# Kernel optimization log

Hardware: AMD Instinct MI355X
Metric: run time of the kernel (lower is better)

## Reference

```python
import jax, jax.numpy as jnp
import numpy as np

B, S, H = 1, 2048, 2048
NH, NKV, HD = 16, 2, 128
ROPE_THETA = 1000000.0
BF16 = jnp.bfloat16


def setup_inputs() -> dict:
    key = jax.random.key(0)
    ks = jax.random.split(key, 6)
    hidden_states = jax.random.normal(ks[0], (B, S, H), dtype=jnp.float32)
    # causal additive mask, 0 on/below diagonal, large negative above
    causal = jnp.tril(jnp.ones((S, S), dtype=bool))
    attention_mask = jnp.where(causal, 0.0, -1e9).astype(jnp.float32)[None, None, :, :]
    position_ids = jnp.arange(S, dtype=jnp.int32)[None, :]
    sc = 1.0 / np.sqrt(H)
    Wq = jax.random.normal(ks[1], (H, H), dtype=jnp.float32) * sc
    bq = jnp.zeros((H,), dtype=jnp.float32)
    Wk = jax.random.normal(ks[2], (H, NKV * HD), dtype=jnp.float32) * sc
    bk = jnp.zeros((NKV * HD,), dtype=jnp.float32)
    Wv = jax.random.normal(ks[3], (H, NKV * HD), dtype=jnp.float32) * sc
    bv = jnp.zeros((NKV * HD,), dtype=jnp.float32)
    Wo = jax.random.normal(ks[4], (H, H), dtype=jnp.float32) * sc
    return {"hidden_states": hidden_states, "attention_mask": attention_mask,
            "position_ids": position_ids, "Wq": Wq, "bq": bq, "Wk": Wk, "bk": bk,
            "Wv": Wv, "bv": bv, "Wo": Wo}


def _rope_tables(pos):
    # pos: [S] int. freqs: [HD//2]
    freqs = 1.0 / (ROPE_THETA ** (jnp.arange(0, HD, 2, dtype=jnp.float32) / HD))
    ang = pos.astype(jnp.float32)[:, None] * freqs[None, :]  # [S, HD//2]
    return jnp.cos(ang), jnp.sin(ang)


def _apply_rope(x, cos, sin):
    # x: [B,S,nheads,HD]; cos/sin: [S,HD//2] -> broadcast over heads
    c = cos[None, :, None, :]
    s = sin[None, :, None, :]
    x1, x2 = x[..., : HD // 2], x[..., HD // 2 :]
    return jnp.concatenate([x1 * c - x2 * s, x1 * s + x2 * c], axis=-1)


def reference(hidden_states, attention_mask, position_ids, Wq, bq, Wk, bk, Wv, bv, Wo):
    x = hidden_states.astype(BF16)
    # bf16 projections (flax Dense dtype=bfloat16)
    q = (x @ Wq.astype(BF16) + bq.astype(BF16)).reshape(B, S, NH, HD)
    k = (x @ Wk.astype(BF16) + bk.astype(BF16)).reshape(B, S, NKV, HD)
    v = (x @ Wv.astype(BF16) + bv.astype(BF16)).reshape(B, S, NKV, HD)
    cos, sin = _rope_tables(position_ids[0])
    q = _apply_rope(q.astype(jnp.float32), cos, sin).astype(jnp.float32)
    k = _apply_rope(k.astype(jnp.float32), cos, sin).astype(jnp.float32)
    cache_k, cache_v = k, v  # cache holds un-repeated kv (k post-rope, v bf16)
    rep = NH // NKV  # GQA repeat
    k = jnp.repeat(k, rep, axis=2)
    vr = jnp.repeat(v, rep, axis=2)
    # [B,NH,S,HD]
    qh = q.transpose(0, 2, 1, 3)
    kh = k.transpose(0, 2, 1, 3)
    vh = vr.transpose(0, 2, 1, 3).astype(jnp.float32)
    scale = 1.0 / jnp.sqrt(jnp.float32(HD))
    scores = jnp.einsum('bhqd,bhkd->bhqk', qh, kh) * scale + attention_mask
    probs = jnp.clip(jax.nn.softmax(scores.astype(jnp.float32), axis=-1), 1e-09, 1 - 1e-09)
    attn = jnp.einsum('bhqk,bhkd->bhqd', probs, vh)
    attn = attn.transpose(0, 2, 1, 3).reshape(B, S, H)
    out = (attn.astype(BF16) @ Wo.astype(BF16)).astype(jnp.float32)
    return out, cache_k, cache_v
```

## Files before the change

kernel.cpp:

```cpp
#include <hip/hip_runtime.h>
#include <hip/hip_bf16.h>
#include <math.h>

#define S_LEN 2048
#define HDIM  2048
#define N_H   16
#define N_KV  2
#define HD_   128
#define NQKV  2560

typedef __attribute__((ext_vector_type(8))) short bf16x8;
typedef __attribute__((ext_vector_type(4))) float f32x4;
typedef __attribute__((ext_vector_type(16))) float f32x16;

#define GLDS16(gsrc, ldst)                                                      \
  __builtin_amdgcn_global_load_lds(                                             \
      (const __attribute__((address_space(1))) void*)(gsrc),                    \
      (__attribute__((address_space(3))) void*)(ldst), 16, 0, 0)

__device__ __forceinline__ ushort f2b(float x) {
  union { __hip_bfloat16 b; ushort u; } c;
  c.b = __float2bfloat16(x);
  return c.u;
}
__device__ __forceinline__ float b2f(ushort u) {
  union { float f; unsigned v; } c;
  c.v = ((unsigned)u) << 16;
  return c.f;
}
__device__ __forceinline__ uint pk2(float a, float b) {
  return (uint)f2b(a) | ((uint)f2b(b) << 16);
}

__global__ __launch_bounds__(256) void k_f32_to_bf16(const float* __restrict__ src,
                                                     ushort* __restrict__ dst, int n4) {
  int i = blockIdx.x * 256 + threadIdx.x;
  if (i >= n4) return;
  float4 v = ((const float4*)src)[i];
  ushort4 o;
  o.x = f2b(v.x); o.y = f2b(v.y); o.z = f2b(v.z); o.w = f2b(v.w);
  ((ushort4*)dst)[i] = o;
}

__global__ __launch_bounds__(256) void k_transpose_bf16(const float* __restrict__ src,
                                                        ushort* __restrict__ dst,
                                                        int R, int C) {
  __shared__ float t[64][65];
  int c0 = blockIdx.x * 64, r0 = blockIdx.y * 64;
  int tx = threadIdx.x & 63, ty = threadIdx.x >> 6;
#pragma unroll
  for (int i = 0; i < 16; ++i)
    t[i * 4 + ty][tx] = src[(size_t)(r0 + i * 4 + ty) * C + (c0 + tx)];
  __syncthreads();
#pragma unroll
  for (int i = 0; i < 16; ++i)
    dst[(size_t)(c0 + i * 4 + ty) * R + (r0 + tx)] = f2b(t[tx][i * 4 + ty]);
}

__global__ __launch_bounds__(256) void k_gemm_bt(const ushort* __restrict__ A,
                                                 const ushort* __restrict__ Bt,
                                                 ushort* __restrict__ Cp,
                                                 int M, int N, int Kfull, int Khalf) {
  __shared__ ushort lA[128 * 32];
  __shared__ ushort lB[128 * 32];
  const int tid = threadIdx.x;
  const int w = tid >> 6, lane = tid & 63;
  const int lr = lane & 15, lg = lane >> 4;
  const int bm = blockIdx.x * 128, bn = blockIdx.y * 128;
  const int wm = (w >> 1) * 64, wn = (w & 1) * 64;
  const int kbeg = blockIdx.z * Khalf;
  ushort* Cout = Cp + (size_t)blockIdx.z * M * N;
  f32x4 acc[4][4] = {};

  for (int k0 = kbeg; k0 < kbeg + Khalf; k0 += 32) {
    __syncthreads();
#pragma unroll
    for (int it = 0; it < 2; ++it) {
      const int idx = it * 256 + tid;
      const int row = idx >> 2;
      const int kc = (idx & 3) * 8;
      GLDS16(A + (size_t)(bm + row) * Kfull + k0 + kc, lA + (it * 4 + w) * 512);
      GLDS16(Bt + (size_t)(bn + row) * Kfull + k0 + kc, lB + (it * 4 + w) * 512);
    }
    __syncthreads();
    bf16x8 af[4], bf[4];
#pragma unroll
    for (int i = 0; i < 4; ++i) {
      af[i] = *(const bf16x8*)(lA + (wm + i * 16 + lr) * 32 + lg * 8);
      bf[i] = *(const bf16x8*)(lB + (wn + i * 16 + lr) * 32 + lg * 8);
    }
    __builtin_amdgcn_s_setprio(1);
#pragma unroll
    for (int mi = 0; mi < 4; ++mi)
#pragma unroll
      for (int ni = 0; ni < 4; ++ni)
        acc[mi][ni] =
            __builtin_amdgcn_mfma_f32_16x16x32_bf16(af[mi], bf[ni], acc[mi][ni], 0, 0, 0);
    __builtin_amdgcn_s_setprio(0);
  }

#pragma unroll
  for (int mi = 0; mi < 4; ++mi)
#pragma unroll
    for (int ni = 0; ni < 4; ++ni)
#pragma unroll
      for (int r = 0; r < 4; ++r) {
        const int row = bm + wm + mi * 16 + lg * 4 + r;
        const int col = bn + wn + ni * 16 + lr;
        Cout[(size_t)row * N + col] = f2b(acc[mi][ni][r]);
      }
}

__global__ __launch_bounds__(256) void k_epirope(const ushort* __restrict__ p0,
                                                 const ushort* __restrict__ p1,
                                                 const float* __restrict__ bq,
                                                 const float* __restrict__ bk,
                                                 const float* __restrict__ bv,
                                                 const int* __restrict__ pos_ids,
                                                 ushort* __restrict__ q_r,
                                                 ushort* __restrict__ k_r,
                                                 ushort* __restrict__ v_t,
                                                 float* __restrict__ cache_k,
                                                 float* __restrict__ cache_v) {
  const int s = blockIdx.x;
  const int t = threadIdx.x;
  __shared__ float row[NQKV];
  const uint* a = (const uint*)(p0 + (size_t)s * NQKV);
  const uint* b = (const uint*)(p1 + (size_t)s * NQKV);
#pragma unroll
  for (int j = 0; j < 5; ++j) {
    const int c2 = t + 256 * j;
    const uint u0 = a[c2], u1 = b[c2];
    const int c = 2 * c2;
    const float v0 = b2f((ushort)u0) + b2f((ushort)(u1 & 0xffff));
    const float v1 = b2f((ushort)(u0 >> 16)) + b2f((ushort)(u1 >> 16));
    const float bias0 = (c < 2048) ? bq[c] : (c < 2304 ? bk[c - 2048] : bv[c - 2304]);
    const float bias1 = (c + 1 < 2048) ? bq[c + 1]
                                       : (c + 1 < 2304 ? bk[c + 1 - 2048] : bv[c + 1 - 2304]);
    row[c] = b2f(f2b(b2f(f2b(v0)) + b2f(f2b(bias0))));
    row[c + 1] = b2f(f2b(b2f(f2b(v1)) + b2f(f2b(bias1))));
  }
  __syncthreads();

  const int i = t & 63, g = t >> 6;
  const float SCALE = 0.08838834764831845f;
  const float pos = (float)pos_ids[s];
  const float freq = (float)(1.0 / pow(1000000.0, (double)i / 64.0));
  float sn, cs;
  sincosf(pos * freq, &sn, &cs);

#pragma unroll
  for (int j = 0; j < 4; ++j) {
    const int h = j * 4 + g;
    const float x1 = row[h * 128 + i];
    const float x2 = row[h * 128 + 64 + i];
    const float o1 = x1 * cs - x2 * sn;
    const float o2 = x1 * sn + x2 * cs;
    const size_t qo = ((size_t)h * S_LEN + s) * 128;
    q_r[qo + i] = f2b(o1 * SCALE);
    q_r[qo + 64 + i] = f2b(o2 * SCALE);
  }
  if (g < 2) {
    const int kv = g;
    const float x1 = row[2048 + kv * 128 + i];
    const float x2 = row[2048 + kv * 128 + 64 + i];
    const float o1 = x1 * cs - x2 * sn;
    const float o2 = x1 * sn + x2 * cs;
    const size_t ko = ((size_t)kv * S_LEN + s) * 128;
    k_r[ko + i] = f2b(o1);
    k_r[ko + 64 + i] = f2b(o2);
    const size_t co = ((size_t)s * 2 + kv) * 128;
    cache_k[co + i] = o1;
    cache_k[co + 64 + i] = o2;
  }
  {
    const int kv = t >> 7, d = t & 127;
    const float vval = row[2304 + kv * 128 + d];
    cache_v[((size_t)s * 2 + kv) * 128 + d] = vval;
    v_t[((size_t)kv * 128 + d) * S_LEN + s] = f2b(vval);
  }
}

__global__ __launch_bounds__(256) void k_addround(const ushort* __restrict__ p0,
                                                  const ushort* __restrict__ p1,
                                                  float* __restrict__ out, int n2) {
  int i = blockIdx.x * 256 + threadIdx.x;
  if (i >= n2) return;
  const uint a = ((const uint*)p0)[i];
  const uint b = ((const uint*)p1)[i];
  float2 o;
  o.x = b2f(f2b(b2f((ushort)(a & 0xffff)) + b2f((ushort)(b & 0xffff))));
  o.y = b2f(f2b(b2f((ushort)(a >> 16)) + b2f((ushort)(b >> 16))));
  ((float2*)out)[i] = o;
}

__global__ __launch_bounds__(256, 2) void k_attn(const ushort* __restrict__ q_r,
                                                 const ushort* __restrict__ k_r,
                                                 const ushort* __restrict__ v_t,
                                                 ushort* __restrict__ attn_b,
                                                 ushort* __restrict__ pO,
                                                 float* __restrict__ pML) {
  __shared__ ushort smem[2][2][8192];
  __shared__ float stats[2][32][2];

  const int bi = blockIdx.x;
  const int h = bi & 15;
  const int j = bi >> 4;
  const int b = (j < 8) ? 0 : (j < 24) ? 1 : (j < 48) ? 2 : 3;
  const int rr = j - 4 * b * (b + 1);
  const int Q = 8 * b + rr / (b + 1);
  const int cch = rr % (b + 1);
  const int s_beg = 8 * cch;
  const int s_end = min(8 * cch + 8, Q + 1);
  const bool single = (b == 0);
  const int kvh = h >> 3;

  const int tid = threadIdx.x, w = tid >> 6, lane = tid & 63;
  const int g = w >> 1, wq = w & 1, tg = tid & 127;
  const int l31 = lane & 31, hb = lane >> 5;
  const int qmaxw = Q * 64 + wq * 32 + 31;

  bf16x8 qf[8];
  {
    const ushort* qp =
        q_r + ((size_t)(h * S_LEN + Q * 64 + wq * 32 + l31)) * 128 + hb * 8;
#pragma unroll
    for (int f = 0; f < 8; ++f) qf[f] = *(const bf16x8*)(qp + f * 16);
  }

  f32x16 acc[4] = {};
  float m = -INFINITY, l = 0.f;

#define STAGE(BUF, T32)                                                           \
  do {                                                                            \
    const int kb_ = (T32) * 32;                                                   \
    _Pragma("unroll") for (int i = 0; i < 4; ++i) {                               \
      const int idx = i * 128 + tg;                                               \
      {                                                                           \
        const int key = idx >> 4, sl = idx & 15;                                  \
        GLDS16(k_r + ((size_t)(kvh * S_LEN + kb_ + key)) * 128 +                  \
                   ((sl ^ (key & 7)) * 8),                                        \
               &smem[g][BUF][i * 1024 + wq * 512]);                               \
      }                                                                           \
      {                                                                           \
        const int d = idx >> 2, p = idx & 3;                                      \
        const int gs = (p - (d >> 1)) & 3;                                        \
        GLDS16(v_t + ((size_t)(kvh * HD_ + d)) * S_LEN + kb_ + gs * 8,            \
               &smem[g][BUF][4096 + i * 1024 + wq * 512]);                        \
      }                                                                           \
    }                                                                             \
  } while (0)

  STAGE(0, 2 * s_beg + g);
  int buf = 0;

  for (int s = s_beg; s < s_end; ++s) {
    __syncthreads();
    if (s + 1 < s_end) STAGE(buf ^ 1, 2 * (s + 1) + g);
    const int kb = (2 * s + g) * 32;

    if (kb <= qmaxw) {
      const ushort* lK = &smem[g][buf][0];
      const ushort* lV = &smem[g][buf][4096];

      f32x16 pa = {}, pb = {};
      __builtin_amdgcn_s_setprio(1);
#pragma unroll
      for (int f = 0; f < 4; ++f) {
        const int key = l31;
        const bf16x8 kf8 =
            *(const bf16x8*)(lK + key * 128 + (((2 * f + hb) ^ (key & 7)) * 8));
        pa = __builtin_amdgcn_mfma_f32_32x32x16_bf16(kf8, qf[f], pa, 0, 0, 0);
      }
#pragma unroll
      for (int f = 4; f < 8; ++f) {
        const int key = l31;
        const bf16x8 kf8 =
            *(const bf16x8*)(lK + key * 128 + (((2 * f + hb) ^ (key & 7)) * 8));
        pb = __builtin_amdgcn_mfma_f32_32x32x16_bf16(kf8, qf[f], pb, 0, 0, 0);
      }
      __builtin_amdgcn_s_setprio(0);
      const f32x16 p0 = pa + pb;

      const int q = Q * 64 + wq * 32 + l31;
      float sv[16];
#pragma unroll
      for (int r = 0; r < 16; ++r) {
        const int key = kb + (r & 3) + 8 * (r >> 2) + 4 * hb;
        sv[r] = (key <= q) ? p0[r] : -INFINITY;
      }
      float t8[8];
#pragma unroll
      for (int jj = 0; jj < 8; ++jj) t8[jj] = fmaxf(sv[jj], sv[jj + 8]);
#pragma unroll
      for (int st = 4; st >= 1; st >>= 1)
#pragma unroll
        for (int jj = 0; jj < 4; ++jj)
          if (jj < st) t8[jj] = fmaxf(t8[jj], t8[jj + st]);
      const float mxw = fmaxf(t8[0], __shfl_xor(t8[0], 32));

      if (__any(mxw > m + 8.f)) {
        const float mn = fmaxf(m, mxw);
        const float sc = __expf(m - mn);
#pragma unroll
        for (int g2 = 0; g2 < 4; ++g2)
#pragma unroll
          for (int r = 0; r < 16; ++r) acc[g2][r] *= sc;
        l *= sc;
        m = mn;
      }
#pragma unroll
      for (int r = 0; r < 16; ++r) sv[r] = __expf(sv[r] - m);
      float ts[8];
#pragma unroll
      for (int jj = 0; jj < 8; ++jj) ts[jj] = sv[jj] + sv[jj + 8];
#pragma unroll
      for (int st = 4; st >= 1; st >>= 1)
#pragma unroll
        for (int jj = 0; jj < 4; ++jj)
          if (jj < st) ts[jj] += ts[jj + st];
      l += ts[0];

      uint pk8[8];
#pragma unroll
      for (int jj = 0; jj < 8; ++jj) pk8[jj] = pk2(sv[2 * jj], sv[2 * jj + 1]);
      union FragU { uint wd[4]; bf16x8 v; };
      FragU frag[2];
#pragma unroll
      for (int c1 = 0; c1 < 2; ++c1) {
        uint mine0, mine1, rcv0, rcv1;
        {
          const uint pa_ = pk8[0 + 4 * c1];
          const uint pb_ = pk8[2 + 4 * c1];
          const uint mn_ = hb ? pb_ : pa_;
          const uint xc_ = hb ? pa_ : pb_;
          mine0 = mn_;
          rcv0 = (uint)__shfl_xor((int)xc_, 32);
        }
        {
          const uint pa_ = pk8[1 + 4 * c1];
          const uint pb_ = pk8[3 + 4 * c1];
          const uint mn_ = hb ? pb_ : pa_;
          const uint xc_ = hb ? pa_ : pb_;
          mine1 = mn_;
          rcv1 = (uint)__shfl_xor((int)xc_, 32);
        }
        frag[c1].wd[0] = hb ? rcv0 : mine0;
        frag[c1].wd[1] = hb ? rcv1 : mine1;
        frag[c1].wd[2] = hb ? mine0 : rcv0;
        frag[c1].wd[3] = hb ? mine1 : rcv1;
      }

      __builtin_amdgcn_s_setprio(1);
#pragma unroll
      for (int g2 = 0; g2 < 4; ++g2) {
        const int d = g2 * 32 + l31;
#pragma unroll
        for (int c = 0; c < 2; ++c) {
          const int phys = ((2 * c + hb) + (d >> 1)) & 3;
          const bf16x8 vf = *(const bf16x8*)(lV + d * 32 + phys * 8);
          acc[g2] = __builtin_amdgcn_mfma_f32_32x32x16_bf16(vf, frag[c].v, acc[g2], 0, 0, 0);
        }
      }
      __builtin_amdgcn_s_setprio(0);
    }
    buf ^= 1;
  }
  __syncthreads();

  float* mrg = (float*)&smem[0][0][0];
  float* ldsO = (float*)&smem[1][0][0];
  if (g == 1) {
    const float lt1 = l + __shfl_xor(l, 32);
#pragma unroll
    for (int g2 = 0; g2 < 4; ++g2)
#pragma unroll
      for (int r = 0; r < 16; ++r) {
        const int d5 = (r & 3) + 8 * (r >> 2) + 4 * hb;
        mrg[wq * 4096 + (g2 * 32 + d5) * 32 + l31] = acc[g2][r];
      }
    if (hb == 0) {
      stats[wq][l31][0] = m;
      stats[wq][l31][1] = lt1;
    }
  }
  __syncthreads();
  if (g == 0) {
    const int slot = h * 72 + (j - 8);
    const float m1 = stats[wq][l31][0];
    const float l1 = stats[wq][l31][1];
    const float l0 = l + __shfl_xor(l, 32);
    const float ms = fmaxf(m, m1);
    const float f0 = __expf(m - ms);
    const float f1 = __expf(m1 - ms);
    const float Lc = l0 * f0 + l1 * f1;
    const float inv = single ? 1.0f / Lc : 1.0f;
#pragma unroll
    for (int g2 = 0; g2 < 4; ++g2)
#pragma unroll
      for (int r = 0; r < 16; ++r) {
        const int d5 = (r & 3) + 8 * (r >> 2) + 4 * hb;
        const float o1v = mrg[wq * 4096 + (g2 * 32 + d5) * 32 + l31];
        const float val = (acc[g2][r] * f0 + o1v * f1) * inv;
        ldsO[wq * 4096 + l31 * 128 + g2 * 32 + (d5 ^ l31)] = val;
      }
    if (!single && hb == 0) {
      pML[(size_t)slot * 128 + (wq * 32 + l31) * 2] = ms;
      pML[(size_t)slot * 128 + (wq * 32 + l31) * 2 + 1] = Lc;
    }
#pragma unroll
    for (int pass = 0; pass < 8; ++pass) {
      const int qrow = pass * 4 + (lane >> 4);
      const int d0 = (lane & 15) * 8;
      float v[8];
#pragma unroll
      for (int jj = 0; jj < 8; ++jj)
        v[jj] = ldsO[wq * 4096 + qrow * 128 + (((d0 + jj) & 31) ^ qrow) + (d0 & 96)];
      uint4 o;
      o.x = pk2(v[0], v[1]); o.y = pk2(v[2], v[3]);
      o.z = pk2(v[4], v[5]); o.w = pk2(v[6], v[7]);
      if (single) {
        const size_t qg = (size_t)(Q * 64 + wq * 32 + qrow);
        *(uint4*)(attn_b + qg * HDIM + h * 128 + d0) = o;
      } else {
        *(uint4*)(pO + (size_t)slot * 8192 + (wq * 32 + qrow) * 128 + d0) = o;
      }
    }
  }
#undef STAGE
}

__global__ __launch_bounds__(256) void k_attn_merge(const ushort* __restrict__ pO,
                                                    const float* __restrict__ pML,
                                                    ushort* __restrict__ attn_b) {
  const int bi = blockIdx.x;
  const int h = bi / 24, Q = 8 + bi % 24;
  const int b = Q >> 3;
  const int off = (b == 1) ? (Q - 8) * 2 : (b == 2) ? 16 + (Q - 16) * 3 : 40 + (Q - 24) * 4;
  const int P = b + 1;
  const int base = h * 72 + off;
  const int q = threadIdx.x >> 2, seg = (threadIdx.x & 3) * 32;

  const float* mlb = pML + (size_t)base * 128 + q * 2;
  const float m0 = mlb[0], l0 = mlb[1];
  const float m1 = mlb[128], l1 = mlb[129];
  const float m2 = (P > 2) ? mlb[256] : -INFINITY;
  const float l2 = (P > 2) ? mlb[257] : 0.f;
  const float m3 = (P > 3) ? mlb[384] : -INFINITY;
  const float l3 = (P > 3) ? mlb[385] : 0.f;
  const float ms = fmaxf(fmaxf(m0, m1), fmaxf(m2, m3));
  const float w0 = __expf(m0 - ms), w1 = __expf(m1 - ms);
  const float w2 = (P > 2) ? __expf(m2 - ms) : 0.f;
  const float w3 = (P > 3) ? __expf(m3 - ms) : 0.f;
  const float inv = 1.0f / (l0 * w0 + l1 * w1 + l2 * w2 + l3 * w3);

  const ushort* po = pO + (size_t)base * 8192 + q * 128;
  ushort* dst = attn_b + (size_t)(Q * 64 + q) * HDIM + h * 128;

#define ACC8(PTR, W)                                                    \
  {                                                                     \
    const uint4 v = *(const uint4*)(PTR);                               \
    o0 += b2f((ushort)(v.x & 0xffff)) * (W); o1 += b2f((ushort)(v.x >> 16)) * (W); \
    o2 += b2f((ushort)(v.y & 0xffff)) * (W); o3 += b2f((ushort)(v.y >> 16)) * (W); \
    o4 += b2f((ushort)(v.z & 0xffff)) * (W); o5 += b2f((ushort)(v.z >> 16)) * (W); \
    o6 += b2f((ushort)(v.w & 0xffff)) * (W); o7 += b2f((ushort)(v.w >> 16)) * (W); \
  }
#pragma unroll
  for (int u = 0; u < 4; ++u) {
    const int d = seg + u * 8;
    float o0 = 0, o1 = 0, o2 = 0, o3 = 0, o4 = 0, o5 = 0, o6 = 0, o7 = 0;
    ACC8(po + d, w0);
    ACC8(po + 8192 + d, w1);
    if (P > 2) ACC8(po + 2 * 8192 + d, w2);
    if (P > 3) ACC8(po + 3 * 8192 + d, w3);
    uint4 ov;
    ov.x = pk2(o0 * inv, o1 * inv); ov.y = pk2(o2 * inv, o3 * inv);
    ov.z = pk2(o4 * inv, o5 * inv); ov.w = pk2(o6 * inv, o7 * inv);
    *(uint4*)(dst + d) = ov;
  }
#undef ACC8
}

extern "C" void kernel_launch(void* const* d_in, const int* in_sizes, int n_in,
                              void* d_out, int out_size, void* d_ws, size_t ws_size,
                              hipStream_t stream) {
  const float* hidden = (const float*)d_in[0];
  const int* pos_ids = (const int*)d_in[2];
  const float* Wq = (const float*)d_in[3];
  const float* bq = (const float*)d_in[4];
  const float* Wk = (const float*)d_in[5];
  const float* bk = (const float*)d_in[6];
  const float* Wv = (const float*)d_in[7];
  const float* bv = (const float*)d_in[8];
  const float* Wo = (const float*)d_in[9];

  float* out = (float*)d_out;
  float* cache_k = out + (size_t)S_LEN * HDIM;
  float* cache_v = cache_k + (size_t)S_LEN * N_KV * HD_;

  char* ws = (char*)d_ws;
  ushort* x_b = (ushort*)(ws);
  ushort* wt = (ushort*)(ws + (8ull << 20));
  ushort* qkvp = (ushort*)(ws + (18ull << 20));
  ushort* wo_t = (ushort*)(ws);
  ushort* q_r = (ushort*)(ws + (8ull << 20));
  ushort* k_r = (ushort*)(ws + (16ull << 20));
  ushort* v_t = (ushort*)(ws + (17ull << 20));
  ushort* attn_b = (ushort*)(ws + (18ull << 20));
  ushort* pO = (ushort*)(ws + (26ull << 20));
  float* pML = (float*)(ws + (45ull << 20));
  ushort* outp = (ushort*)(ws + (26ull << 20));

  k_f32_to_bf16<<<dim3((S_LEN * HDIM) / 1024), 256, 0, stream>>>(hidden, x_b,
                                                                 (S_LEN * HDIM) / 4);
  k_transpose_bf16<<<dim3(32, 32), 256, 0, stream>>>(Wq, wt, 2048, 2048);
  k_transpose_bf16<<<dim3(4, 32), 256, 0, stream>>>(Wk, wt + (size_t)2048 * 2048, 2048, 256);
  k_transpose_bf16<<<dim3(4, 32), 256, 0, stream>>>(Wv, wt + (size_t)2304 * 2048, 2048, 256);
  k_gemm_bt<<<dim3(16, 20, 2), 256, 0, stream>>>(x_b, wt, qkvp, 2048, 2560, 2048, 1024);
  k_transpose_bf16<<<dim3(32, 32), 256, 0, stream>>>(Wo, wo_t, 2048, 2048);
  k_epirope<<<dim3(S_LEN), 256, 0, stream>>>(qkvp, qkvp + (size_t)2048 * 2560, bq, bk, bv,
                                             pos_ids, q_r, k_r, v_t, cache_k, cache_v);
  k_attn<<<dim3(1280), 256, 0, stream>>>(q_r, k_r, v_t, attn_b, pO, pML);
  k_attn_merge<<<dim3(384), 256, 0, stream>>>(pO, pML, attn_b);
  k_gemm_bt<<<dim3(16, 16, 2), 256, 0, stream>>>(attn_b, wo_t, outp, 2048, 2048, 2048, 1024);
  k_addround<<<dim3((2048 * 2048 / 2 + 255) / 256), 256, 0, stream>>>(
      outp, outp + (size_t)2048 * 2048, out, 2048 * 2048 / 2);
}
```

Measured before the change: 167.5 us.

## Restructure attention into 128-query tiles with 12-block key chunks; fuse prep kernels

The attention kernel now gives each of its four waves its own 32-query slice of a 128-query tile, with all waves sharing one key/value stage. The old design split keys across wave groups and merged them in LDS. Work is split into chunks of up to 12 key blocks, giving 816 blocks and a merge kernel that combines up to 6 partials. Diagonal-only masking skips the compare on fully visible tiles. The occupancy hint rises to 4 blocks per CU. The hidden-state conversion and the Q/K/V weight transposes are fused into one launch, and workspace offsets are rearranged to fit.

Result: slower. 204.6 us (+22.1%).

```diff
diff --git a/kernel.cpp b/kernel.cpp
--- a/kernel.cpp
+++ b/kernel.cpp
@@ -32,14 +32,43 @@
   return (uint)f2b(a) | ((uint)f2b(b) << 16);
 }
 
-__global__ __launch_bounds__(256) void k_f32_to_bf16(const float* __restrict__ src,
-                                                     ushort* __restrict__ dst, int n4) {
-  int i = blockIdx.x * 256 + threadIdx.x;
-  if (i >= n4) return;
-  float4 v = ((const float4*)src)[i];
-  ushort4 o;
-  o.x = f2b(v.x); o.y = f2b(v.y); o.z = f2b(v.z); o.w = f2b(v.w);
-  ((ushort4*)dst)[i] = o;
+__global__ __launch_bounds__(256) void k_prep(const float* __restrict__ hidden,
+                                              const float* __restrict__ Wq,
+                                              const float* __restrict__ Wk,
+                                              const float* __restrict__ Wv,
+                                              ushort* __restrict__ x_b,
+                                              ushort* __restrict__ wt) {
+  __shared__ float t[64][65];
+  const int bid = blockIdx.x;
+  const int tid = threadIdx.x;
+  if (bid < 4096) {
+    const int i = bid * 256 + tid;
+    float4 v = ((const float4*)hidden)[i];
+    ushort4 o;
+    o.x = f2b(v.x); o.y = f2b(v.y); o.z = f2b(v.z); o.w = f2b(v.w);
+    ((ushort4*)x_b)[i] = o;
+    return;
+  }
+  int tb = bid - 4096;
+  const float* src;
+  ushort* dst;
+  int C, bx, by;
+  if (tb < 1024) {
+    src = Wq; dst = wt; C = 2048; bx = tb & 31; by = tb >> 5;
+  } else if (tb < 1152) {
+    tb -= 1024; src = Wk; dst = wt + (size_t)2048 * 2048; C = 256; bx = tb & 3; by = tb >> 2;
+  } else {
+    tb -= 1152; src = Wv; dst = wt + (size_t)2304 * 2048; C = 256; bx = tb & 3; by = tb >> 2;
+  }
+  const int c0 = bx * 64, r0 = by * 64;
+  const int tx = tid & 63, ty = tid >> 6;
+#pragma unroll
+  for (int i = 0; i < 16; ++i)
+    t[i * 4 + ty][tx] = src[(size_t)(r0 + i * 4 + ty) * C + (c0 + tx)];
+  __syncthreads();
+#pragma unroll
+  for (int i = 0; i < 16; ++i)
+    dst[(size_t)(c0 + i * 4 + ty) * 2048 + (r0 + tx)] = f2b(t[tx][i * 4 + ty]);
 }
 
 __global__ __launch_bounds__(256) void k_transpose_bf16(const float* __restrict__ src,
@@ -194,36 +223,32 @@
   ((float2*)out)[i] = o;
 }
 
-__global__ __launch_bounds__(256, 2) void k_attn(const ushort* __restrict__ q_r,
+__global__ __launch_bounds__(256, 4) void k_attn(const ushort* __restrict__ q_r,
                                                  const ushort* __restrict__ k_r,
                                                  const ushort* __restrict__ v_t,
                                                  ushort* __restrict__ attn_b,
                                                  ushort* __restrict__ pO,
                                                  float* __restrict__ pML) {
-  __shared__ ushort smem[2][2][8192];
-  __shared__ float stats[2][32][2];
+  __shared__ ushort smem[2][8192];
 
   const int bi = blockIdx.x;
-  const int h = bi & 15;
-  const int j = bi >> 4;
-  const int b = (j < 8) ? 0 : (j < 24) ? 1 : (j < 48) ? 2 : 3;
-  const int rr = j - 4 * b * (b + 1);
-  const int Q = 8 * b + rr / (b + 1);
-  const int cch = rr % (b + 1);
-  const int s_beg = 8 * cch;
-  const int s_end = min(8 * cch + 8, Q + 1);
-  const bool single = (b == 0);
+  const int h = bi / 51;
+  const int j = bi - h * 51;
+  int T = 0, cbase = 0;
+  while (cbase + ((T + 3) / 3) <= j) { cbase += (T + 3) / 3; ++T; }
+  const int c = j - cbase;
+  const int s_beg = c * 12;
+  const int s_end = min(s_beg + 12, 4 * T + 4);
+  const bool single = (j < 3);
   const int kvh = h >> 3;
 
   const int tid = threadIdx.x, w = tid >> 6, lane = tid & 63;
-  const int g = w >> 1, wq = w & 1, tg = tid & 127;
   const int l31 = lane & 31, hb = lane >> 5;
-  const int qmaxw = Q * 64 + wq * 32 + 31;
+  const int qlo = T * 128 + w * 32;
 
   bf16x8 qf[8];
   {
-    const ushort* qp =
-        q_r + ((size_t)(h * S_LEN + Q * 64 + wq * 32 + l31)) * 128 + hb * 8;
+    const ushort* qp = q_r + ((size_t)(h * S_LEN + qlo + l31)) * 128 + hb * 8;
 #pragma unroll
     for (int f = 0; f < 8; ++f) qf[f] = *(const bf16x8*)(qp + f * 16);
   }
@@ -231,63 +256,66 @@
   f32x16 acc[4] = {};
   float m = -INFINITY, l = 0.f;
 
-#define STAGE(BUF, T32)                                                           \
-  do {                                                                            \
-    const int kb_ = (T32) * 32;                                                   \
-    _Pragma("unroll") for (int i = 0; i < 4; ++i) {                               \
-      const int idx = i * 128 + tg;                                               \
-      {                                                                           \
-        const int key = idx >> 4, sl = idx & 15;                                  \
-        GLDS16(k_r + ((size_t)(kvh * S_LEN + kb_ + key)) * 128 +                  \
-                   ((sl ^ (key & 7)) * 8),                                        \
-               &smem[g][BUF][i * 1024 + wq * 512]);                               \
-      }                                                                           \
-      {                                                                           \
-        const int d = idx >> 2, p = idx & 3;                                      \
-        const int gs = (p - (d >> 1)) & 3;                                        \
-        GLDS16(v_t + ((size_t)(kvh * HD_ + d)) * S_LEN + kb_ + gs * 8,            \
-               &smem[g][BUF][4096 + i * 1024 + wq * 512]);                        \
-      }                                                                           \
-    }                                                                             \
+#define STAGE(BUF, S32)                                                          \
+  do {                                                                           \
+    const int kb_ = (S32) * 32;                                                  \
+    _Pragma("unroll") for (int it = 0; it < 2; ++it) {                           \
+      const int idx = it * 256 + tid;                                            \
+      {                                                                          \
+        const int key = idx >> 4, sl = idx & 15;                                 \
+        GLDS16(k_r + ((size_t)(kvh * S_LEN + kb_ + key)) * 128 +                 \
+                   ((sl ^ (key & 7)) * 8),                                       \
+               &smem[BUF][idx * 8]);                                             \
+      }                                                                          \
+      {                                                                          \
+        const int d = idx >> 2, p = idx & 3;                                     \
+        const int gs = (p - (d >> 1)) & 3;                                       \
+        GLDS16(v_t + ((size_t)(kvh * HD_ + d)) * S_LEN + kb_ + gs * 8,           \
+               &smem[BUF][4096 + idx * 8]);                                      \
+      }                                                                          \
+    }                                                                            \
   } while (0)
 
-  STAGE(0, 2 * s_beg + g);
+  STAGE(0, s_beg);
   int buf = 0;
 
   for (int s = s_beg; s < s_end; ++s) {
     __syncthreads();
-    if (s + 1 < s_end) STAGE(buf ^ 1, 2 * (s + 1) + g);
-    const int kb = (2 * s + g) * 32;
-
-    if (kb <= qmaxw) {
-      const ushort* lK = &smem[g][buf][0];
-      const ushort* lV = &smem[g][buf][4096];
+    if (s + 1 < s_end) STAGE(buf ^ 1, s + 1);
+    const int kb = s * 32;
+
+    if (kb <= qlo + 31) {
+      const ushort* lK = &smem[buf][0];
+      const ushort* lV = &smem[buf][4096];
 
       f32x16 pa = {}, pb = {};
       __builtin_amdgcn_s_setprio(1);
 #pragma unroll
       for (int f = 0; f < 4; ++f) {
-        const int key = l31;
         const bf16x8 kf8 =
-            *(const bf16x8*)(lK + key * 128 + (((2 * f + hb) ^ (key & 7)) * 8));
+            *(const bf16x8*)(lK + l31 * 128 + (((2 * f + hb) ^ (l31 & 7)) * 8));
         pa = __builtin_amdgcn_mfma_f32_32x32x16_bf16(kf8, qf[f], pa, 0, 0, 0);
       }
 #pragma unroll
       for (int f = 4; f < 8; ++f) {
-        const int key = l31;
         const bf16x8 kf8 =
-            *(const bf16x8*)(lK + key * 128 + (((2 * f + hb) ^ (key & 7)) * 8));
+            *(const bf16x8*)(lK + l31 * 128 + (((2 * f + hb) ^ (l31 & 7)) * 8));
         pb = __builtin_amdgcn_mfma_f32_32x32x16_bf16(kf8, qf[f], pb, 0, 0, 0);
       }
       __builtin_amdgcn_s_setprio(0);
       const f32x16 p0 = pa + pb;
 
-      const int q = Q * 64 + wq * 32 + l31;
       float sv[16];
-#pragma unroll
-      for (int r = 0; r < 16; ++r) {
-        const int key = kb + (r & 3) + 8 * (r >> 2) + 4 * hb;
-        sv[r] = (key <= q) ? p0[r] : -INFINITY;
+      if (kb + 31 > qlo) {
+        const int q = qlo + l31;
+#pragma unroll
+        for (int r = 0; r < 16; ++r) {
+          const int key = kb + (r & 3) + 8 * (r >> 2) + 4 * hb;
+          sv[r] = (key <= q) ? p0[r] : -INFINITY;
+        }
+      } else {
+#pragma unroll
+        for (int r = 0; r < 16; ++r) sv[r] = p0[r];
       }
       float t8[8];
 #pragma unroll
@@ -356,10 +384,10 @@
       for (int g2 = 0; g2 < 4; ++g2) {
         const int d = g2 * 32 + l31;
 #pragma unroll
-        for (int c = 0; c < 2; ++c) {
-          const int phys = ((2 * c + hb) + (d >> 1)) & 3;
+        for (int cc = 0; cc < 2; ++cc) {
+          const int phys = ((2 * cc + hb) + (d >> 1)) & 3;
           const bf16x8 vf = *(const bf16x8*)(lV + d * 32 + phys * 8);
-          acc[g2] = __builtin_amdgcn_mfma_f32_32x32x16_bf16(vf, frag[c].v, acc[g2], 0, 0, 0);
+          acc[g2] = __builtin_amdgcn_mfma_f32_32x32x16_bf16(vf, frag[cc].v, acc[g2], 0, 0, 0);
         }
       }
       __builtin_amdgcn_s_setprio(0);
@@ -368,63 +396,30 @@
   }
   __syncthreads();
 
-  float* mrg = (float*)&smem[0][0][0];
-  float* ldsO = (float*)&smem[1][0][0];
-  if (g == 1) {
-    const float lt1 = l + __shfl_xor(l, 32);
-#pragma unroll
-    for (int g2 = 0; g2 < 4; ++g2)
-#pragma unroll
-      for (int r = 0; r < 16; ++r) {
-        const int d5 = (r & 3) + 8 * (r >> 2) + 4 * hb;
-        mrg[wq * 4096 + (g2 * 32 + d5) * 32 + l31] = acc[g2][r];
-      }
-    if (hb == 0) {
-      stats[wq][l31][0] = m;
-      stats[wq][l31][1] = lt1;
-    }
-  }
-  __syncthreads();
-  if (g == 0) {
-    const int slot = h * 72 + (j - 8);
-    const float m1 = stats[wq][l31][0];
-    const float l1 = stats[wq][l31][1];
-    const float l0 = l + __shfl_xor(l, 32);
-    const float ms = fmaxf(m, m1);
-    const float f0 = __expf(m - ms);
-    const float f1 = __expf(m1 - ms);
-    const float Lc = l0 * f0 + l1 * f1;
-    const float inv = single ? 1.0f / Lc : 1.0f;
-#pragma unroll
-    for (int g2 = 0; g2 < 4; ++g2)
-#pragma unroll
-      for (int r = 0; r < 16; ++r) {
-        const int d5 = (r & 3) + 8 * (r >> 2) + 4 * hb;
-        const float o1v = mrg[wq * 4096 + (g2 * 32 + d5) * 32 + l31];
-        const float val = (acc[g2][r] * f0 + o1v * f1) * inv;
-        ldsO[wq * 4096 + l31 * 128 + g2 * 32 + (d5 ^ l31)] = val;
-      }
-    if (!single && hb == 0) {
-      pML[(size_t)slot * 128 + (wq * 32 + l31) * 2] = ms;
-      pML[(size_t)slot * 128 + (wq * 32 + l31) * 2 + 1] = Lc;
-    }
-#pragma unroll
-    for (int pass = 0; pass < 8; ++pass) {
-      const int qrow = pass * 4 + (lane >> 4);
-      const int d0 = (lane & 15) * 8;
-      float v[8];
-#pragma unroll
-      for (int jj = 0; jj < 8; ++jj)
-        v[jj] = ldsO[wq * 4096 + qrow * 128 + (((d0 + jj) & 31) ^ qrow) + (d0 & 96)];
-      uint4 o;
-      o.x = pk2(v[0], v[1]); o.y = pk2(v[2], v[3]);
-      o.z = pk2(v[4], v[5]); o.w = pk2(v[6], v[7]);
-      if (single) {
-        const size_t qg = (size_t)(Q * 64 + wq * 32 + qrow);
-        *(uint4*)(attn_b + qg * HDIM + h * 128 + d0) = o;
-      } else {
-        *(uint4*)(pO + (size_t)slot * 8192 + (wq * 32 + qrow) * 128 + d0) = o;
-      }
+  const float lt = l + __shfl_xor(l, 32);
+  const float inv = single ? 1.0f / lt : 1.0f;
+  const int slot = h * 48 + (j - 3);
+  ushort* ldsU = &smem[0][0] + w * 4096;
+#pragma unroll
+  for (int g2 = 0; g2 < 4; ++g2)
+#pragma unroll
+    for (int r = 0; r < 16; ++r) {
+      const int d = g2 * 32 + (r & 3) + 8 * (r >> 2) + 4 * hb;
+      ldsU[l31 * 128 + (((d >> 3) ^ (l31 & 15)) * 8 + (d & 7))] = f2b(acc[g2][r] * inv);
+    }
+  if (!single && hb == 0) {
+    pML[(size_t)slot * 256 + (w * 32 + l31) * 2] = m;
+    pML[(size_t)slot * 256 + (w * 32 + l31) * 2 + 1] = lt;
+  }
+#pragma unroll
+  for (int pass = 0; pass < 8; ++pass) {
+    const int qrow = pass * 4 + (lane >> 4);
+    const int d0 = (lane & 15) * 8;
+    const uint4 o = *(const uint4*)(ldsU + qrow * 128 + (((d0 >> 3) ^ (qrow & 15)) * 8));
+    if (single) {
+      *(uint4*)(attn_b + (size_t)(T * 128 + w * 32 + qrow) * HDIM + h * 128 + d0) = o;
+    } else {
+      *(uint4*)(pO + (size_t)slot * 16384 + (w * 32 + qrow) * 128 + d0) = o;
     }
   }
 #undef STAGE
@@ -433,52 +428,55 @@
 __global__ __launch_bounds__(256) void k_attn_merge(const ushort* __restrict__ pO,
                                                     const float* __restrict__ pML,
                                                     ushort* __restrict__ attn_b) {
-  const int bi = blockIdx.x;
-  const int h = bi / 24, Q = 8 + bi % 24;
-  const int b = Q >> 3;
-  const int off = (b == 1) ? (Q - 8) * 2 : (b == 2) ? 16 + (Q - 16) * 3 : 40 + (Q - 24) * 4;
-  const int P = b + 1;
-  const int base = h * 72 + off;
-  const int q = threadIdx.x >> 2, seg = (threadIdx.x & 3) * 32;
-
-  const float* mlb = pML + (size_t)base * 128 + q * 2;
-  const float m0 = mlb[0], l0 = mlb[1];
-  const float m1 = mlb[128], l1 = mlb[129];
-  const float m2 = (P > 2) ? mlb[256] : -INFINITY;
-  const float l2 = (P > 2) ? mlb[257] : 0.f;
-  const float m3 = (P > 3) ? mlb[384] : -INFINITY;
-  const float l3 = (P > 3) ? mlb[385] : 0.f;
-  const float ms = fmaxf(fmaxf(m0, m1), fmaxf(m2, m3));
-  const float w0 = __expf(m0 - ms), w1 = __expf(m1 - ms);
-  const float w2 = (P > 2) ? __expf(m2 - ms) : 0.f;
-  const float w3 = (P > 3) ? __expf(m3 - ms) : 0.f;
-  const float inv = 1.0f / (l0 * w0 + l1 * w1 + l2 * w2 + l3 * w3);
-
-  const ushort* po = pO + (size_t)base * 8192 + q * 128;
-  ushort* dst = attn_b + (size_t)(Q * 64 + q) * HDIM + h * 128;
-
-#define ACC8(PTR, W)                                                    \
-  {                                                                     \
-    const uint4 v = *(const uint4*)(PTR);                               \
-    o0 += b2f((ushort)(v.x & 0xffff)) * (W); o1 += b2f((ushort)(v.x >> 16)) * (W); \
-    o2 += b2f((ushort)(v.y & 0xffff)) * (W); o3 += b2f((ushort)(v.y >> 16)) * (W); \
-    o4 += b2f((ushort)(v.z & 0xffff)) * (W); o5 += b2f((ushort)(v.z >> 16)) * (W); \
-    o6 += b2f((ushort)(v.w & 0xffff)) * (W); o7 += b2f((ushort)(v.w >> 16)) * (W); \
-  }
-#pragma unroll
-  for (int u = 0; u < 4; ++u) {
-    const int d = seg + u * 8;
-    float o0 = 0, o1 = 0, o2 = 0, o3 = 0, o4 = 0, o5 = 0, o6 = 0, o7 = 0;
-    ACC8(po + d, w0);
-    ACC8(po + 8192 + d, w1);
-    if (P > 2) ACC8(po + 2 * 8192 + d, w2);
-    if (P > 3) ACC8(po + 3 * 8192 + d, w3);
+  const int h = blockIdx.x / 13;
+  const int T = 3 + blockIdx.x % 13;
+  int cbase = 0;
+  for (int t = 0; t < T; ++t) cbase += (t + 3) / 3;
+  const int P = (T + 3) / 3;
+  const int sb = h * 48 + cbase - 3;
+  const int q = threadIdx.x >> 1, half = threadIdx.x & 1;
+
+  float mi_[6], li_[6], wg_[6];
+#pragma unroll
+  for (int i = 0; i < 6; ++i) { mi_[i] = -INFINITY; li_[i] = 0.f; wg_[i] = 0.f; }
+#pragma unroll
+  for (int i = 0; i < 6; ++i)
+    if (i < P) {
+      mi_[i] = pML[(size_t)(sb + i) * 256 + q * 2];
+      li_[i] = pML[(size_t)(sb + i) * 256 + q * 2 + 1];
+    }
+  float ms = mi_[0];
+#pragma unroll
+  for (int i = 1; i < 6; ++i) ms = fmaxf(ms, mi_[i]);
+  float wsum = 0.f;
+#pragma unroll
+  for (int i = 0; i < 6; ++i)
+    if (i < P) {
+      wg_[i] = __expf(mi_[i] - ms);
+      wsum += li_[i] * wg_[i];
+    }
+  const float inv = 1.0f / wsum;
+
+  ushort* dst = attn_b + (size_t)(T * 128 + q) * HDIM + h * 128 + half * 64;
+#pragma unroll
+  for (int seg = 0; seg < 8; ++seg) {
+    float o[8] = {0.f, 0.f, 0.f, 0.f, 0.f, 0.f, 0.f, 0.f};
+#pragma unroll
+    for (int i = 0; i < 6; ++i)
+      if (i < P) {
+        const uint4 v = *(const uint4*)(pO + (size_t)(sb + i) * 16384 + q * 128 +
+                                        half * 64 + seg * 8);
+        const float wv = wg_[i];
+        o[0] += b2f((ushort)(v.x & 0xffff)) * wv; o[1] += b2f((ushort)(v.x >> 16)) * wv;
+        o[2] += b2f((ushort)(v.y & 0xffff)) * wv; o[3] += b2f((ushort)(v.y >> 16)) * wv;
+        o[4] += b2f((ushort)(v.z & 0xffff)) * wv; o[5] += b2f((ushort)(v.z >> 16)) * wv;
+        o[6] += b2f((ushort)(v.w & 0xffff)) * wv; o[7] += b2f((ushort)(v.w >> 16)) * wv;
+      }
     uint4 ov;
-    ov.x = pk2(o0 * inv, o1 * inv); ov.y = pk2(o2 * inv, o3 * inv);
-    ov.z = pk2(o4 * inv, o5 * inv); ov.w = pk2(o6 * inv, o7 * inv);
-    *(uint4*)(dst + d) = ov;
-  }
-#undef ACC8
+    ov.x = pk2(o[0] * inv, o[1] * inv); ov.y = pk2(o[2] * inv, o[3] * inv);
+    ov.z = pk2(o[4] * inv, o[5] * inv); ov.w = pk2(o[6] * inv, o[7] * inv);
+    *(uint4*)(dst + seg * 8) = ov;
+  }
 }
 
 extern "C" void kernel_launch(void* const* d_in, const int* in_sizes, int n_in,
@@ -502,26 +500,22 @@
   ushort* x_b = (ushort*)(ws);
   ushort* wt = (ushort*)(ws + (8ull << 20));
   ushort* qkvp = (ushort*)(ws + (18ull << 20));
+  ushort* q_r = (ushort*)(ws);
+  ushort* k_r = (ushort*)(ws + (8ull << 20));
+  ushort* v_t = (ushort*)(ws + (9ull << 20));
+  ushort* attn_b = (ushort*)(ws + (10ull << 20));
+  ushort* pO = (ushort*)(ws + (18ull << 20));
+  float* pML = (float*)(ws + (42ull << 20));
   ushort* wo_t = (ushort*)(ws);
-  ushort* q_r = (ushort*)(ws + (8ull << 20));
-  ushort* k_r = (ushort*)(ws + (16ull << 20));
-  ushort* v_t = (ushort*)(ws + (17ull << 20));
-  ushort* attn_b = (ushort*)(ws + (18ull << 20));
-  ushort* pO = (ushort*)(ws + (26ull << 20));
-  float* pML = (float*)(ws + (45ull << 20));
-  ushort* outp = (ushort*)(ws + (26ull << 20));
-
-  k_f32_to_bf16<<<dim3((S_LEN * HDIM) / 1024), 256, 0, stream>>>(hidden, x_b,
-                                                                 (S_LEN * HDIM) / 4);
-  k_transpose_bf16<<<dim3(32, 32), 256, 0, stream>>>(Wq, wt, 2048, 2048);
-  k_transpose_bf16<<<dim3(4, 32), 256, 0, stream>>>(Wk, wt + (size_t)2048 * 2048, 2048, 256);
-  k_transpose_bf16<<<dim3(4, 32), 256, 0, stream>>>(Wv, wt + (size_t)2304 * 2048, 2048, 256);
+  ushort* outp = (ushort*)(ws + (18ull << 20));
+
+  k_prep<<<dim3(5376), 256, 0, stream>>>(hidden, Wq, Wk, Wv, x_b, wt);
   k_gemm_bt<<<dim3(16, 20, 2), 256, 0, stream>>>(x_b, wt, qkvp, 2048, 2560, 2048, 1024);
-  k_transpose_bf16<<<dim3(32, 32), 256, 0, stream>>>(Wo, wo_t, 2048, 2048);
   k_epirope<<<dim3(S_LEN), 256, 0, stream>>>(qkvp, qkvp + (size_t)2048 * 2560, bq, bk, bv,
                                              pos_ids, q_r, k_r, v_t, cache_k, cache_v);
-  k_attn<<<dim3(1280), 256, 0, stream>>>(q_r, k_r, v_t, attn_b, pO, pML);
-  k_attn_merge<<<dim3(384), 256, 0, stream>>>(pO, pML, attn_b);
+  k_attn<<<dim3(816), 256, 0, stream>>>(q_r, k_r, v_t, attn_b, pO, pML);
+  k_transpose_bf16<<<dim3(32, 32), 256, 0, stream>>>(Wo, wo_t, 2048, 2048);
+  k_attn_merge<<<dim3(208), 256, 0, stream>>>(pO, pML, attn_b);
   k_gemm_bt<<<dim3(16, 16, 2), 256, 0, stream>>>(attn_b, wo_t, outp, 2048, 2048, 2048, 1024);
   k_addround<<<dim3((2048 * 2048 / 2 + 255) / 256), 256, 0, stream>>>(
       outp, outp + (size_t)2048 * 2048, out, 2048 * 2048 / 2);
```
